# Optimization experiments

Hardware: AMD Instinct MI355X
Metric: run time of the kernel (lower is better)

Reference implementation:

```python
import jax, jax.numpy as jnp
import numpy as np
import math

DIM = 1024
NUMHEADS = 16
HEAD_DIM = DIM // NUMHEADS
B, N = 4, 1024


def setup_inputs() -> dict:
    key = jax.random.key(0)
    ks = jax.random.split(key, 12)
    x = jax.random.normal(ks[0], (B, N, DIM), dtype=jnp.float32)
    decaymask = jax.random.uniform(ks[1], (NUMHEADS, N, N), dtype=jnp.float32)
    s = 1.0 / math.sqrt(DIM)
    wq = jax.random.normal(ks[2], (DIM, DIM), dtype=jnp.float32) * s
    bq = jnp.zeros((DIM,), dtype=jnp.float32)
    wk = jax.random.normal(ks[3], (DIM, DIM), dtype=jnp.float32) * s
    bk = jnp.zeros((DIM,), dtype=jnp.float32)
    wv = jax.random.normal(ks[4], (DIM, DIM), dtype=jnp.float32) * s
    bv = jnp.zeros((DIM,), dtype=jnp.float32)
    wo = jax.random.normal(ks[5], (DIM, DIM), dtype=jnp.float32) * s
    bo = jnp.zeros((DIM,), dtype=jnp.float32)
    return {"x": x, "decaymask": decaymask, "wq": wq, "bq": bq, "wk": wk,
            "bk": bk, "wv": wv, "bv": bv, "wo": wo, "bo": bo}


def reference(x, decaymask, wq, bq, wk, bk, wv, bv, wo, bo):
    Bx, Nx, D = x.shape
    # projections (torch Linear: x @ W^T + b)
    q = x @ wq.T + bq
    k = x @ wk.T + bk
    v = x @ wv.T + bv
    # [B, H, N, Hd]
    q = q.reshape(Bx, Nx, NUMHEADS, HEAD_DIM).transpose(0, 2, 1, 3)
    k = k.reshape(Bx, Nx, NUMHEADS, HEAD_DIM).transpose(0, 2, 1, 3)
    v = v.reshape(Bx, Nx, NUMHEADS, HEAD_DIM).transpose(0, 2, 1, 3)
    scores = jnp.einsum('bhqd,bhkd->bhqk', q, k) / math.sqrt(HEAD_DIM)
    scores = scores * decaymask[None]  # multiplicative decay mask before softmax
    attn = jax.nn.softmax(scores, axis=-1)
    out = jnp.einsum('bhqk,bhkd->bhqd', attn, v)
    out = out.transpose(0, 2, 1, 3).reshape(Bx, Nx, D)
    return out @ wo.T + bo
```

## Files before the change

### kernel.cpp

```cpp
#include <hip/hip_runtime.h>
#include <hip/hip_bf16.h>
#include <math.h>

typedef __bf16 bf16;
typedef __bf16 bf16x8 __attribute__((ext_vector_type(8)));
typedef __bf16 bf16x4 __attribute__((ext_vector_type(4)));
typedef float f32x4 __attribute__((ext_vector_type(4)));
typedef unsigned short u16;
typedef u16 u16x8 __attribute__((ext_vector_type(8)));

#define SEQ 1024
#define DIMSZ 1024
#define NHEADS 16
#define HEADDIM 64
#define BATCH 4
#define MTOK (BATCH * SEQ)

#define QSCALE 0.180336880f

typedef __attribute__((address_space(1))) const unsigned char gas_u8;
typedef __attribute__((address_space(3))) unsigned char las_u8;
__device__ __forceinline__ void gload16(const void* g, void* l) {
    __builtin_amdgcn_global_load_lds((const gas_u8*)g, (las_u8*)l, 16, 0, 0);
}

__device__ __forceinline__ void cvt_store(const float4 v, bf16* dst, int e0, float scale) {
    int row = e0 >> 10, col = e0 & 1023;
    int col2 = (col & ~63) | (col & 7) | (((((col >> 3) & 7) ^ (row & 7))) << 3);
    bf16x4 o;
    o[0] = (bf16)(v.x * scale);
    o[1] = (bf16)(v.y * scale);
    o[2] = (bf16)(v.z * scale);
    o[3] = (bf16)(v.w * scale);
    *reinterpret_cast<bf16x4*>(&dst[(size_t)row * 1024 + col2]) = o;
}

__global__ void cvt_all(const float4* __restrict__ x,
                        const float4* __restrict__ wq, const float4* __restrict__ wk,
                        const float4* __restrict__ wv, const float4* __restrict__ wo,
                        bf16* __restrict__ xb, bf16* __restrict__ wqkvb,
                        bf16* __restrict__ wob) {
    int i = blockIdx.x * blockDim.x + threadIdx.x;
    if (i < 1048576) {
        cvt_store(x[i], xb, i << 2, 1.f);
    } else {
        int li = i - 1048576;
        int mat = li >> 18, lj = li & 262143;
        const float4* s = (mat == 0) ? wq : (mat == 1) ? wk : (mat == 2) ? wv : wo;
        bf16* d = (mat < 3) ? (wqkvb + (size_t)mat * 1024 * 1024) : wob;
        cvt_store(s[lj], d, lj << 2, (mat == 0) ? QSCALE : 1.f);
    }
}

__device__ __forceinline__ bf16x8 fragswz(const bf16* base, int row, int kb) {
    return *reinterpret_cast<const bf16x8*>(
        reinterpret_cast<const char*>(base) + row * 128 + (kb ^ ((row & 7) << 4)));
}

#define LDT 72

template <int WN, int OUT_F32>
__global__ __launch_bounds__(256) void gemm_glds(
    const bf16* __restrict__ A, const bf16* __restrict__ Bm,
    const float* __restrict__ b0, const float* __restrict__ b1, const float* __restrict__ b2,
    float s0, void* __restrict__ Cv, int M, int N, int K)
{
    __shared__ __align__(16) bf16 As[128 * 64];
    __shared__ __align__(16) bf16 Bs[WN * 32 * 64];

    const int BN = WN * 32;
    const int nbn = N / BN;
    const int wrk = (blockIdx.x & 7) * ((int)gridDim.x >> 3) + (blockIdx.x >> 3);
    const int bm = wrk / nbn, bn = wrk % nbn;
    const int m0 = bm << 7, n0 = bn * BN;
    const int tid = threadIdx.x, lane = tid & 63, wid = tid >> 6;
    const int wr = wid >> 1, wc = wid & 1;
    const int lq = lane & 15, g = lane >> 4;

    f32x4 acc[4][WN];
    #pragma unroll
    for (int m = 0; m < 4; ++m)
        #pragma unroll
        for (int n = 0; n < WN; ++n)
            acc[m][n] = (f32x4){0.f, 0.f, 0.f, 0.f};

    for (int kt = 0; kt < K; kt += 64) {
        #pragma unroll
        for (int i = 0; i < 4; ++i) {
            int rb = wid * 32 + i * 8;
            gload16(&A[(size_t)(m0 + rb + (lane >> 3)) * K + kt + ((lane & 7) << 3)],
                    &As[rb * 64]);
        }
        #pragma unroll
        for (int i = 0; i < WN; ++i) {
            int rb = wid * (WN * 8) + i * 8;
            gload16(&Bm[(size_t)(n0 + rb + (lane >> 3)) * K + kt + ((lane & 7) << 3)],
                    &Bs[rb * 64]);
        }
        __syncthreads();

        bf16x8 af[4][2], bfr[WN][2];
        #pragma unroll
        for (int m = 0; m < 4; ++m)
            #pragma unroll
            for (int h2 = 0; h2 < 2; ++h2)
                af[m][h2] = fragswz(As, wr * 64 + m * 16 + lq, h2 * 64 + g * 16);
        #pragma unroll
        for (int n = 0; n < WN; ++n)
            #pragma unroll
            for (int h2 = 0; h2 < 2; ++h2)
                bfr[n][h2] = fragswz(Bs, wc * (WN * 16) + n * 16 + lq, h2 * 64 + g * 16);

        #pragma unroll
        for (int m = 0; m < 4; ++m)
            #pragma unroll
            for (int n = 0; n < WN; ++n)
                #pragma unroll
                for (int h2 = 0; h2 < 2; ++h2)
                    acc[m][n] = __builtin_amdgcn_mfma_f32_16x16x32_bf16(
                        af[m][h2], bfr[n][h2], acc[m][n], 0, 0, 0);
        __syncthreads();
    }

    const int seg = n0 >> 10;
    const float* bp = (seg == 0) ? b0 : ((seg == 1) ? b1 : b2);
    const float bsc = (seg == 0) ? s0 : 1.f;

    #pragma unroll
    for (int m = 0; m < 4; ++m) {
        #pragma unroll
        for (int n = 0; n < WN; ++n) {
            int rbase = m0 + wr * 64 + m * 16 + (g << 2);
            int col = n0 + wc * (WN * 16) + n * 16 + lq;
            float bv = bp[col - (seg << 10)] * bsc;
            #pragma unroll
            for (int r = 0; r < 4; ++r) {
                float v = acc[m][n][r] + bv;
                if (OUT_F32)
                    ((float*)Cv)[(size_t)(rbase + r) * N + col] = v;
                else
                    ((bf16*)Cv)[(size_t)(rbase + r) * N + col] = (bf16)v;
            }
        }
    }
}

struct KVRegs { bf16x8 k0, k1; u16x8 v0, v1; };

__device__ __forceinline__ void issue_loads(KVRegs& r, const bf16* qkv, int brow,
                                            int koff, int voff, int tid) {
    const int rK = tid >> 3, o8 = (tid & 7) << 3;
    r.k0 = *reinterpret_cast<const bf16x8*>(&qkv[(size_t)(brow + rK) * 3072 + koff + o8]);
    r.k1 = *reinterpret_cast<const bf16x8*>(&qkv[(size_t)(brow + rK + 32) * 3072 + koff + o8]);
    const int rV = rK << 1;
    r.v0 = *reinterpret_cast<const u16x8*>(&qkv[(size_t)(brow + rV) * 3072 + voff + o8]);
    r.v1 = *reinterpret_cast<const u16x8*>(&qkv[(size_t)(brow + rV + 1) * 3072 + voff + o8]);
}

__device__ __forceinline__ void write_stage(const KVRegs& r, bf16* Kb, bf16* Vb, int tid) {
    const int rK = tid >> 3, o = tid & 7;
    char* kb = reinterpret_cast<char*>(Kb);
    int kx = (o << 4) ^ ((rK & 7) << 4);
    *reinterpret_cast<bf16x8*>(kb + rK * 128 + kx) = r.k0;
    *reinterpret_cast<bf16x8*>(kb + (rK + 32) * 128 + kx) = r.k1;
    const int rV = rK << 1;
    char* vb = reinterpret_cast<char*>(Vb);
    #pragma unroll
    for (int j = 0; j < 8; ++j) {
        int d = (o << 3) + j;
        int byteo = (d * 144 + rV * 2) ^ (o << 4);
        unsigned int w = (unsigned int)r.v0[j] | ((unsigned int)r.v1[j] << 16);
        *reinterpret_cast<unsigned int*>(vb + byteo) = w;
    }
}

__device__ __forceinline__ void compute_stage(
    const bf16* Kb, const bf16* Vb, bf16* Psw,
    const float4 (&mreg)[4], const bf16x8 (&aqb)[2],
    f32x4& lacc, f32x4 (&oacc)[4], int lane)
{
    const int lq = lane & 15, g = lane >> 4;
    f32x4 sacc[4];
    #pragma unroll
    for (int ct = 0; ct < 4; ++ct) sacc[ct] = (f32x4){0.f, 0.f, 0.f, 0.f};
    #pragma unroll
    for (int ct = 0; ct < 4; ++ct)
        #pragma unroll
        for (int h2 = 0; h2 < 2; ++h2)
            sacc[ct] = __builtin_amdgcn_mfma_f32_16x16x32_bf16(
                fragswz(Kb, ct * 16 + lq, h2 * 64 + g * 16), aqb[h2], sacc[ct], 0, 0, 0);

    #pragma unroll
    for (int ct = 0; ct < 4; ++ct) {
        float p0 = __builtin_exp2f(sacc[ct][0] * mreg[ct].x);
        float p1 = __builtin_exp2f(sacc[ct][1] * mreg[ct].y);
        float p2 = __builtin_exp2f(sacc[ct][2] * mreg[ct].z);
        float p3 = __builtin_exp2f(sacc[ct][3] * mreg[ct].w);
        lacc[0] += p0; lacc[1] += p1; lacc[2] += p2; lacc[3] += p3;
        bf16x4 pbv;
        pbv[0] = (bf16)p0; pbv[1] = (bf16)p1; pbv[2] = (bf16)p2; pbv[3] = (bf16)p3;
        *reinterpret_cast<bf16x4*>(&Psw[lq * LDT + ct * 16 + (g << 2)]) = pbv;
    }

    const char* vb = reinterpret_cast<const char*>(Vb);
    #pragma unroll
    for (int ot = 0; ot < 4; ++ot) {
        #pragma unroll
        for (int h2 = 0; h2 < 2; ++h2) {
            int d = ot * 16 + lq;
            int byteo = (d * 144 + (h2 * 32 + g * 8) * 2) ^ (((d >> 3) & 7) << 4);
            bf16x8 vf = *reinterpret_cast<const bf16x8*>(vb + byteo);
            bf16x8 pf = *reinterpret_cast<const bf16x8*>(&Psw[lq * LDT + h2 * 32 + g * 8]);
            oacc[ot] = __builtin_amdgcn_mfma_f32_16x16x32_bf16(vf, pf, oacc[ot], 0, 0, 0);
        }
    }
}

__global__ __launch_bounds__(256) void attn_kernel(
    const bf16* __restrict__ qkv, const float* __restrict__ mask, bf16* __restrict__ Og)
{
    __shared__ __align__(16) bf16 Kbuf[2][2][64 * 64];
    __shared__ __align__(16) bf16 Vbuf[2][2][64 * LDT];
    __shared__ __align__(16) bf16 Ps[4][16 * LDT];

    const int bid = blockIdx.x;
    const int xcd = bid & 7, slot = bid >> 3;
    const int pg = xcd * 32 + (slot >> 1);
    const int bp = slot & 1;
    const int h = pg >> 4, qblk = pg & 15;

    const int tid = threadIdx.x, lane = tid & 63, wid = tid >> 6;
    const int lq = lane & 15, g = lane >> 4;
    const int q = (qblk << 6) + wid * 16 + lq;
    const int koff = 1024 + h * HEADDIM, voff = 2048 + h * HEADDIM, qoff = h * HEADDIM;
    const int b0 = bp * 2, b1 = bp * 2 + 1;
    const float* mh = mask + (size_t)h * SEQ * SEQ + (size_t)q * SEQ;

    bf16x8 aq[2][2];
    #pragma unroll
    for (int bi = 0; bi < 2; ++bi)
        #pragma unroll
        for (int h2 = 0; h2 < 2; ++h2)
            aq[bi][h2] = *reinterpret_cast<const bf16x8*>(
                &qkv[(size_t)((b0 + bi) * SEQ + q) * 3072 + qoff + h2 * 32 + g * 8]);

    f32x4 lacc[2] = {};
    f32x4 oacc[2][4] = {};

    KVRegs s0, s1;
    issue_loads(s0, qkv, b0 * SEQ, koff, voff, tid);
    issue_loads(s1, qkv, b1 * SEQ, koff, voff, tid);
    write_stage(s0, Kbuf[0][0], Vbuf[0][0], tid);
    write_stage(s1, Kbuf[1][0], Vbuf[1][0], tid);
    issue_loads(s0, qkv, b0 * SEQ + 64, koff, voff, tid);
    issue_loads(s1, qkv, b1 * SEQ + 64, koff, voff, tid);
    float4 mcur[4], mnxt[4];
    #pragma unroll
    for (int ct = 0; ct < 4; ++ct) {
        mcur[ct] = *reinterpret_cast<const float4*>(&mh[ct * 16 + (g << 2)]);
        mnxt[ct] = *reinterpret_cast<const float4*>(&mh[64 + ct * 16 + (g << 2)]);
    }
    __syncthreads();

    for (int t = 0; t < 16; ++t) {
        int pp = t & 1, np = pp ^ 1;
        if (t < 15) {
            write_stage(s0, Kbuf[0][np], Vbuf[0][np], tid);
            write_stage(s1, Kbuf[1][np], Vbuf[1][np], tid);
        }
        if (t < 14) {
            issue_loads(s0, qkv, b0 * SEQ + (t + 2) * 64, koff, voff, tid);
            issue_loads(s1, qkv, b1 * SEQ + (t + 2) * 64, koff, voff, tid);
        }
        compute_stage(Kbuf[0][pp], Vbuf[0][pp], Ps[wid], mcur, aq[0], lacc[0], oacc[0], lane);
        compute_stage(Kbuf[1][pp], Vbuf[1][pp], Ps[wid], mcur, aq[1], lacc[1], oacc[1], lane);
        #pragma unroll
        for (int ct = 0; ct < 4; ++ct) mcur[ct] = mnxt[ct];
        if (t < 14)
            #pragma unroll
            for (int ct = 0; ct < 4; ++ct)
                mnxt[ct] = *reinterpret_cast<const float4*>(&mh[(t + 2) * 64 + ct * 16 + (g << 2)]);
        __syncthreads();
    }

    #pragma unroll
    for (int bi = 0; bi < 2; ++bi) {
        float lsum = lacc[bi][0] + lacc[bi][1] + lacc[bi][2] + lacc[bi][3];
        lsum += __shfl_xor(lsum, 16, 64);
        lsum += __shfl_xor(lsum, 32, 64);
        float inv = 1.f / lsum;
        #pragma unroll
        for (int ot = 0; ot < 4; ++ot) {
            bf16x4 o;
            o[0] = (bf16)(oacc[bi][ot][0] * inv);
            o[1] = (bf16)(oacc[bi][ot][1] * inv);
            o[2] = (bf16)(oacc[bi][ot][2] * inv);
            o[3] = (bf16)(oacc[bi][ot][3] * inv);
            int lcol = ot * 16 + (g << 2);
            int chunk = (lcol >> 3) ^ (q & 7);
            int col = h * HEADDIM + (chunk << 3) + (lcol & 7);
            *reinterpret_cast<bf16x4*>(
                &Og[(size_t)((b0 + bi) * SEQ + q) * DIMSZ + col]) = o;
        }
    }
}

extern "C" void kernel_launch(void* const* d_in, const int* in_sizes, int n_in,
                              void* d_out, int out_size, void* d_ws, size_t ws_size,
                              hipStream_t stream) {
    const float* x    = (const float*)d_in[0];
    const float* mask = (const float*)d_in[1];
    const float* wq   = (const float*)d_in[2];
    const float* bq   = (const float*)d_in[3];
    const float* wk   = (const float*)d_in[4];
    const float* bk   = (const float*)d_in[5];
    const float* wv   = (const float*)d_in[6];
    const float* bv   = (const float*)d_in[7];
    const float* wo   = (const float*)d_in[8];
    const float* bo   = (const float*)d_in[9];
    float* out = (float*)d_out;

    char* ws = (char*)d_ws;
    bf16* xb    = (bf16*)ws; ws += (size_t)MTOK * DIMSZ * 2;
    bf16* wqkvb = (bf16*)ws; ws += (size_t)3 * DIMSZ * DIMSZ * 2;
    bf16* wob   = (bf16*)ws; ws += (size_t)DIMSZ * DIMSZ * 2;
    bf16* qkv   = (bf16*)ws; ws += (size_t)MTOK * 3 * DIMSZ * 2;
    bf16* aob   = (bf16*)ws; ws += (size_t)MTOK * DIMSZ * 2;

    cvt_all<<<(2 * 1048576) / 256, 256, 0, stream>>>(
        (const float4*)x, (const float4*)wq, (const float4*)wk,
        (const float4*)wv, (const float4*)wo, xb, wqkvb, wob);

    gemm_glds<4, 0><<<(MTOK / 128) * (3 * DIMSZ / 128), 256, 0, stream>>>(
        xb, wqkvb, bq, bk, bv, QSCALE, qkv, MTOK, 3 * DIMSZ, DIMSZ);

    attn_kernel<<<512, 256, 0, stream>>>(qkv, mask, aob);

    gemm_glds<2, 1><<<(MTOK / 128) * (DIMSZ / 64), 256, 0, stream>>>(
        aob, wob, bo, bo, bo, 1.f, out, MTOK, DIMSZ, DIMSZ);
}
```

Before: 116.1 us.

## Restructure attention blocks to one batch with 8 waves over 128 queries

Each attention block now processes a single batch element with 512 threads (8 waves covering 128 query rows), where before it used 256 threads covering 64 queries across two batch elements. K/V tile loading is split so the first half of the threads loads K and the second half loads and transposes V. This halves per-thread register state and LDS per query and spreads the load work, aiming for higher occupancy. The trade-off is that the decay mask is no longer reused across two batches inside one block, so mask traffic relies on the cache more.

Result: faster. 108.3 us (median of 2 runs) (-6.7%).

```diff
diff --git a/kernel.cpp b/kernel.cpp
--- a/kernel.cpp
+++ b/kernel.cpp
@@ -145,32 +145,42 @@
     }
 }
 
-struct KVRegs { bf16x8 k0, k1; u16x8 v0, v1; };
-
-__device__ __forceinline__ void issue_loads(KVRegs& r, const bf16* qkv, int brow,
-                                            int koff, int voff, int tid) {
-    const int rK = tid >> 3, o8 = (tid & 7) << 3;
-    r.k0 = *reinterpret_cast<const bf16x8*>(&qkv[(size_t)(brow + rK) * 3072 + koff + o8]);
-    r.k1 = *reinterpret_cast<const bf16x8*>(&qkv[(size_t)(brow + rK + 32) * 3072 + koff + o8]);
-    const int rV = rK << 1;
-    r.v0 = *reinterpret_cast<const u16x8*>(&qkv[(size_t)(brow + rV) * 3072 + voff + o8]);
-    r.v1 = *reinterpret_cast<const u16x8*>(&qkv[(size_t)(brow + rV + 1) * 3072 + voff + o8]);
-}
-
-__device__ __forceinline__ void write_stage(const KVRegs& r, bf16* Kb, bf16* Vb, int tid) {
-    const int rK = tid >> 3, o = tid & 7;
-    char* kb = reinterpret_cast<char*>(Kb);
-    int kx = (o << 4) ^ ((rK & 7) << 4);
-    *reinterpret_cast<bf16x8*>(kb + rK * 128 + kx) = r.k0;
-    *reinterpret_cast<bf16x8*>(kb + (rK + 32) * 128 + kx) = r.k1;
-    const int rV = rK << 1;
-    char* vb = reinterpret_cast<char*>(Vb);
-    #pragma unroll
-    for (int j = 0; j < 8; ++j) {
-        int d = (o << 3) + j;
-        int byteo = (d * 144 + rV * 2) ^ (o << 4);
-        unsigned int w = (unsigned int)r.v0[j] | ((unsigned int)r.v1[j] << 16);
-        *reinterpret_cast<unsigned int*>(vb + byteo) = w;
+struct KV { bf16x8 a, b; };
+
+__device__ __forceinline__ void issue_kv(KV& r, const bf16* qkv, int brow,
+                                         int koff, int voff, int tid) {
+    if (tid < 256) {
+        const int rK = tid >> 3, o8 = (tid & 7) << 3;
+        r.a = *reinterpret_cast<const bf16x8*>(&qkv[(size_t)(brow + rK) * 3072 + koff + o8]);
+        r.b = *reinterpret_cast<const bf16x8*>(&qkv[(size_t)(brow + rK + 32) * 3072 + koff + o8]);
+    } else {
+        const int t2 = tid - 256;
+        const int kp = t2 >> 3, o8 = (t2 & 7) << 3;
+        r.a = *reinterpret_cast<const bf16x8*>(&qkv[(size_t)(brow + 2 * kp) * 3072 + voff + o8]);
+        r.b = *reinterpret_cast<const bf16x8*>(&qkv[(size_t)(brow + 2 * kp + 1) * 3072 + voff + o8]);
+    }
+}
+
+__device__ __forceinline__ void write_kv(const KV& r, bf16* Kb, bf16* Vb, int tid) {
+    if (tid < 256) {
+        const int rK = tid >> 3, o = tid & 7;
+        char* kb = reinterpret_cast<char*>(Kb);
+        int kx = (o << 4) ^ ((rK & 7) << 4);
+        *reinterpret_cast<bf16x8*>(kb + rK * 128 + kx) = r.a;
+        *reinterpret_cast<bf16x8*>(kb + (rK + 32) * 128 + kx) = r.b;
+    } else {
+        const int t2 = tid - 256;
+        const int kp = t2 >> 3, o = t2 & 7;
+        const u16x8 v0 = *reinterpret_cast<const u16x8*>(&r.a);
+        const u16x8 v1 = *reinterpret_cast<const u16x8*>(&r.b);
+        char* vb = reinterpret_cast<char*>(Vb);
+        #pragma unroll
+        for (int j = 0; j < 8; ++j) {
+            int d = (o << 3) + j;
+            int byteo = (d * 144 + kp * 4) ^ (o << 4);
+            unsigned int w = (unsigned int)v0[j] | ((unsigned int)v1[j] << 16);
+            *reinterpret_cast<unsigned int*>(vb + byteo) = w;
+        }
     }
 }
 
@@ -216,44 +226,39 @@
     }
 }
 
-__global__ __launch_bounds__(256) void attn_kernel(
+__global__ __launch_bounds__(512, 4) void attn_kernel(
     const bf16* __restrict__ qkv, const float* __restrict__ mask, bf16* __restrict__ Og)
 {
-    __shared__ __align__(16) bf16 Kbuf[2][2][64 * 64];
-    __shared__ __align__(16) bf16 Vbuf[2][2][64 * LDT];
-    __shared__ __align__(16) bf16 Ps[4][16 * LDT];
+    __shared__ __align__(16) bf16 Kbuf[2][64 * 64];
+    __shared__ __align__(16) bf16 Vbuf[2][64 * LDT];
+    __shared__ __align__(16) bf16 Ps[8][16 * LDT];
 
     const int bid = blockIdx.x;
     const int xcd = bid & 7, slot = bid >> 3;
-    const int pg = xcd * 32 + (slot >> 1);
-    const int bp = slot & 1;
-    const int h = pg >> 4, qblk = pg & 15;
+    const int b = slot & 3;
+    const int pg = xcd * 16 + (slot >> 2);
+    const int h = pg >> 3, qblk = pg & 7;
 
     const int tid = threadIdx.x, lane = tid & 63, wid = tid >> 6;
     const int lq = lane & 15, g = lane >> 4;
-    const int q = (qblk << 6) + wid * 16 + lq;
+    const int q = (qblk << 7) + wid * 16 + lq;
+    const int brow = b * SEQ;
     const int koff = 1024 + h * HEADDIM, voff = 2048 + h * HEADDIM, qoff = h * HEADDIM;
-    const int b0 = bp * 2, b1 = bp * 2 + 1;
     const float* mh = mask + (size_t)h * SEQ * SEQ + (size_t)q * SEQ;
 
-    bf16x8 aq[2][2];
-    #pragma unroll
-    for (int bi = 0; bi < 2; ++bi)
-        #pragma unroll
-        for (int h2 = 0; h2 < 2; ++h2)
-            aq[bi][h2] = *reinterpret_cast<const bf16x8*>(
-                &qkv[(size_t)((b0 + bi) * SEQ + q) * 3072 + qoff + h2 * 32 + g * 8]);
-
-    f32x4 lacc[2] = {};
-    f32x4 oacc[2][4] = {};
-
-    KVRegs s0, s1;
-    issue_loads(s0, qkv, b0 * SEQ, koff, voff, tid);
-    issue_loads(s1, qkv, b1 * SEQ, koff, voff, tid);
-    write_stage(s0, Kbuf[0][0], Vbuf[0][0], tid);
-    write_stage(s1, Kbuf[1][0], Vbuf[1][0], tid);
-    issue_loads(s0, qkv, b0 * SEQ + 64, koff, voff, tid);
-    issue_loads(s1, qkv, b1 * SEQ + 64, koff, voff, tid);
+    bf16x8 aq[2];
+    #pragma unroll
+    for (int h2 = 0; h2 < 2; ++h2)
+        aq[h2] = *reinterpret_cast<const bf16x8*>(
+            &qkv[(size_t)(brow + q) * 3072 + qoff + h2 * 32 + g * 8]);
+
+    f32x4 lacc = {};
+    f32x4 oacc[4] = {};
+
+    KV s;
+    issue_kv(s, qkv, brow, koff, voff, tid);
+    write_kv(s, Kbuf[0], Vbuf[0], tid);
+    issue_kv(s, qkv, brow + 64, koff, voff, tid);
     float4 mcur[4], mnxt[4];
     #pragma unroll
     for (int ct = 0; ct < 4; ++ct) {
@@ -264,16 +269,9 @@
 
     for (int t = 0; t < 16; ++t) {
         int pp = t & 1, np = pp ^ 1;
-        if (t < 15) {
-            write_stage(s0, Kbuf[0][np], Vbuf[0][np], tid);
-            write_stage(s1, Kbuf[1][np], Vbuf[1][np], tid);
-        }
-        if (t < 14) {
-            issue_loads(s0, qkv, b0 * SEQ + (t + 2) * 64, koff, voff, tid);
-            issue_loads(s1, qkv, b1 * SEQ + (t + 2) * 64, koff, voff, tid);
-        }
-        compute_stage(Kbuf[0][pp], Vbuf[0][pp], Ps[wid], mcur, aq[0], lacc[0], oacc[0], lane);
-        compute_stage(Kbuf[1][pp], Vbuf[1][pp], Ps[wid], mcur, aq[1], lacc[1], oacc[1], lane);
+        if (t < 15) write_kv(s, Kbuf[np], Vbuf[np], tid);
+        if (t < 14) issue_kv(s, qkv, brow + (t + 2) * 64, koff, voff, tid);
+        compute_stage(Kbuf[pp], Vbuf[pp], Ps[wid], mcur, aq, lacc, oacc, lane);
         #pragma unroll
         for (int ct = 0; ct < 4; ++ct) mcur[ct] = mnxt[ct];
         if (t < 14)
@@ -283,25 +281,21 @@
         __syncthreads();
     }
 
-    #pragma unroll
-    for (int bi = 0; bi < 2; ++bi) {
-        float lsum = lacc[bi][0] + lacc[bi][1] + lacc[bi][2] + lacc[bi][3];
-        lsum += __shfl_xor(lsum, 16, 64);
-        lsum += __shfl_xor(lsum, 32, 64);
-        float inv = 1.f / lsum;
-        #pragma unroll
-        for (int ot = 0; ot < 4; ++ot) {
-            bf16x4 o;
-            o[0] = (bf16)(oacc[bi][ot][0] * inv);
-            o[1] = (bf16)(oacc[bi][ot][1] * inv);
-            o[2] = (bf16)(oacc[bi][ot][2] * inv);
-            o[3] = (bf16)(oacc[bi][ot][3] * inv);
-            int lcol = ot * 16 + (g << 2);
-            int chunk = (lcol >> 3) ^ (q & 7);
-            int col = h * HEADDIM + (chunk << 3) + (lcol & 7);
-            *reinterpret_cast<bf16x4*>(
-                &Og[(size_t)((b0 + bi) * SEQ + q) * DIMSZ + col]) = o;
-        }
+    float lsum = lacc[0] + lacc[1] + lacc[2] + lacc[3];
+    lsum += __shfl_xor(lsum, 16, 64);
+    lsum += __shfl_xor(lsum, 32, 64);
+    float inv = 1.f / lsum;
+    #pragma unroll
+    for (int ot = 0; ot < 4; ++ot) {
+        bf16x4 o;
+        o[0] = (bf16)(oacc[ot][0] * inv);
+        o[1] = (bf16)(oacc[ot][1] * inv);
+        o[2] = (bf16)(oacc[ot][2] * inv);
+        o[3] = (bf16)(oacc[ot][3] * inv);
+        int lcol = ot * 16 + (g << 2);
+        int chunk = (lcol >> 3) ^ (q & 7);
+        int col = h * HEADDIM + (chunk << 3) + (lcol & 7);
+        *reinterpret_cast<bf16x4*>(&Og[(size_t)(brow + q) * DIMSZ + col]) = o;
     }
 }
 
@@ -334,7 +328,7 @@
     gemm_glds<4, 0><<<(MTOK / 128) * (3 * DIMSZ / 128), 256, 0, stream>>>(
         xb, wqkvb, bq, bk, bv, QSCALE, qkv, MTOK, 3 * DIMSZ, DIMSZ);
 
-    attn_kernel<<<512, 256, 0, stream>>>(qkv, mask, aob);
+    attn_kernel<<<512, 512, 0, stream>>>(qkv, mask, aob);
 
     gemm_glds<2, 1><<<(MTOK / 128) * (DIMSZ / 64), 256, 0, stream>>>(
         aob, wob, bo, bo, bo, 1.f, out, MTOK, DIMSZ, DIMSZ);
```
